# Kernel optimization log

Hardware: AMD Instinct MI355X
Metric: run time of the kernel (lower is better)

Reference implementation:

```python
import jax, jax.numpy as jnp
import numpy as np

B, G, P, H = 32, 5000, 5000, 64
N = B * G
E_CO, E_GG = 1600000, 100000

def _bn(x, g, b):
    # BatchNorm1d in training mode: biased batch stats, eps=1e-5
    m = x.mean(0); v = x.var(0)
    return g * (x - m) * jax.lax.rsqrt(v + 1e-5) + b

def _renorm(t):
    # nn.Embedding(max_norm=True) -> rows renormed to L2 norm <= 1
    n = jnp.linalg.norm(t, axis=1, keepdims=True)
    return t * jnp.minimum(1.0, 1.0 / jnp.maximum(n, 1e-12))

def _sgconv(x, src, dst, w, W, b):
    # SGConv(K=1): gcn_norm (self-loops w=1, symmetric deg norm) spmm, then Linear
    n = x.shape[0]
    sl = jnp.arange(n)
    s = jnp.concatenate([src, sl]); d = jnp.concatenate([dst, sl])
    ww = jnp.concatenate([w, jnp.ones((n,), x.dtype)])
    deg = jax.ops.segment_sum(ww, d, num_segments=n)
    dinv = jnp.where(deg > 0, jax.lax.rsqrt(deg), 0.0)
    coef = dinv[s] * ww * dinv[d]
    agg = jax.ops.segment_sum(coef[:, None] * x[s], d, num_segments=n)
    return agg @ W.T + b

def _mlp3(x, W, b, g, bt):
    # MLP([h,h,h]): Lin-BN-ReLU-Lin-BN (trailing ReLU stripped by [:-1])
    h = jax.nn.relu(_bn(x @ W[0].T + b[0], g[0], bt[0]))
    return _bn(h @ W[1].T + b[1], g[1], bt[1])

def _gears(x, pert_idx, ei_co, w_co, ei_go, w_go, ei_bg, w_bg,
           gene_tab, pos_tab, go_tab, bg_tab, bn_g, bn_b, sg_W, sg_b,
           mlp_W, mlp_b, mlp_g, mlp_bt,
           rec_W1, rec_b1, rec_g1, rec_bt1, rec_W2, rec_b2, rec_g2, rec_bt2,
           indv_w1, indv_b1,
           cg_W1, cg_b1, cg_g1, cg_bt1, cg_W2, cg_b2, cg_g2, cg_bt2,
           indv_w2, indv_b2):
    nb = pert_idx.shape[0]
    ng = gene_tab.shape[0]
    emb = jnp.tile(_renorm(gene_tab), (nb, 1))                     # [B*G,H]
    base = jax.nn.relu(_bn(emb, bn_g[0], bn_b[0]))                 # bn_emb + emb_trans
    pos = jnp.tile(_renorm(pos_tab), (nb, 1))
    pos = _sgconv(pos, ei_co[0], ei_co[1], w_co, sg_W[0], sg_b[0]) # 1 gene-pos GNN layer, no trailing relu
    base = base + 0.2 * pos
    base = _mlp3(base, mlp_W[1], mlp_b[1], mlp_g[1], mlp_bt[1])    # emb_trans_v2
    pgo = _sgconv(_renorm(go_tab), ei_go[0], ei_go[1], w_go, sg_W[1], sg_b[1])
    pbg = _sgconv(_renorm(bg_tab), ei_bg[0], ei_bg[1], w_bg, sg_W[2], sg_b[2])
    pglob = _mlp3(pgo + pbg, mlp_W[0], mlp_b[0], mlp_g[0], mlp_bt[0])  # pert_emb_comb_trans
    base = base.reshape(nb, ng, -1)
    # one valid pert per graph -> pert_track reduces to a gather; pert_fuse then broadcast-add
    emb_total = _mlp3(pglob[pert_idx], mlp_W[2], mlp_b[2], mlp_g[2], mlp_bt[2])  # [B,H]
    base = base + emb_total[:, None, :]
    base = base.reshape(nb * ng, -1)
    base = jax.nn.relu(_bn(base, bn_g[1], bn_b[1]))                # bn_pert_base + transform
    h = jax.nn.relu(_bn(base @ rec_W1.T + rec_b1, rec_g1, rec_bt1))
    out = _bn(h @ rec_W2.T + rec_b2, rec_g2, rec_bt2).reshape(nb, ng, -1)
    w1 = jnp.einsum('bgh,gh->bg', out, indv_w1) + indv_b1          # per-gene decoder 1
    cg = jax.nn.relu(_bn(w1 @ cg_W1.T + cg_b1, cg_g1, cg_bt1))
    cg = _bn(cg @ cg_W2.T + cg_b2, cg_g2, cg_bt2)                  # cross_gene_state [B,H]
    cat = jnp.concatenate([w1[..., None], jnp.broadcast_to(cg[:, None, :], (nb, ng, cg.shape[-1]))], -1)
    out2 = jnp.einsum('bgk,gk->bg', cat, indv_w2) + indv_b2        # per-gene decoder 2
    return out2 + x.reshape(nb, ng)

def setup_inputs():
    ks = jax.random.split(jax.random.key(0), 48)
    rn = lambda i, sh, s=0.05: jax.random.normal(ks[i], sh, jnp.float32) * s
    return {
        "x": rn(0, (N,), 1.0),
        "pert_idx": jax.random.randint(ks[1], (B,), 0, P),
        "ei_co": jax.random.randint(ks[2], (2, E_CO), 0, N),
        "w_co": jax.random.uniform(ks[3], (E_CO,), jnp.float32),
        "ei_go": jax.random.randint(ks[4], (2, E_GG), 0, P),
        "w_go": jax.random.uniform(ks[5], (E_GG,), jnp.float32),
        "ei_bg": jax.random.randint(ks[6], (2, E_GG), 0, P),
        "w_bg": jax.random.uniform(ks[7], (E_GG,), jnp.float32),
        "gene_tab": rn(8, (G, H), 1.0),
        "pos_tab": rn(9, (G, H), 1.0),
        "go_tab": rn(10, (P, H), 1.0),
        "bg_tab": rn(11, (P, H), 1.0),
        "bn_g": jnp.ones((2, H)), "bn_b": jnp.zeros((2, H)),
        "sg_W": rn(12, (3, H, H)), "sg_b": jnp.zeros((3, H)),
        "mlp_W": rn(13, (3, 2, H, H)), "mlp_b": jnp.zeros((3, 2, H)),
        "mlp_g": jnp.ones((3, 2, H)), "mlp_bt": jnp.zeros((3, 2, H)),
        "rec_W1": rn(14, (2 * H, H)), "rec_b1": jnp.zeros((2 * H,)),
        "rec_g1": jnp.ones((2 * H,)), "rec_bt1": jnp.zeros((2 * H,)),
        "rec_W2": rn(15, (H, 2 * H)), "rec_b2": jnp.zeros((H,)),
        "rec_g2": jnp.ones((H,)), "rec_bt2": jnp.zeros((H,)),
        "indv_w1": rn(16, (G, H)), "indv_b1": rn(17, (G,)),
        "cg_W1": rn(18, (H, G), 0.01), "cg_b1": jnp.zeros((H,)),
        "cg_g1": jnp.ones((H,)), "cg_bt1": jnp.zeros((H,)),
        "cg_W2": rn(19, (H, H)), "cg_b2": jnp.zeros((H,)),
        "cg_g2": jnp.ones((H,)), "cg_bt2": jnp.zeros((H,)),
        "indv_w2": rn(20, (G, H + 1)), "indv_b2": rn(21, (G,)),
    }

def reference(x, pert_idx, ei_co, w_co, ei_go, w_go, ei_bg, w_bg,
              gene_tab, pos_tab, go_tab, bg_tab, bn_g, bn_b, sg_W, sg_b,
              mlp_W, mlp_b, mlp_g, mlp_bt,
              rec_W1, rec_b1, rec_g1, rec_bt1, rec_W2, rec_b2, rec_g2, rec_bt2,
              indv_w1, indv_b1,
              cg_W1, cg_b1, cg_g1, cg_bt1, cg_W2, cg_b2, cg_g2, cg_bt2,
              indv_w2, indv_b2):
    return _gears(x, pert_idx, ei_co, w_co, ei_go, w_go, ei_bg, w_bg,
                  gene_tab, pos_tab, go_tab, bg_tab, bn_g, bn_b, sg_W, sg_b,
                  mlp_W, mlp_b, mlp_g, mlp_bt,
                  rec_W1, rec_b1, rec_g1, rec_bt1, rec_W2, rec_b2, rec_g2, rec_bt2,
                  indv_w1, indv_b1,
                  cg_W1, cg_b1, cg_g1, cg_bt1, cg_W2, cg_b2, cg_g2, cg_bt2,
                  indv_w2, indv_b2)
```

## Files before the change

### kernel.cpp

```cpp
#include <hip/hip_runtime.h>

typedef unsigned int u32;
typedef unsigned short u16;

constexpr int Gn  = 5000;
constexpr int Bn  = 32;
constexpr int Pn  = 5000;
constexpr int Nn  = Bn * Gn;
constexpr int ECO = 1600000;
constexpr int EGG = 100000;
constexpr int NTILES = Nn / 128;
constexpr int PTILES = 40;
constexpr int NBK = 625;
constexpr int EPB2 = ECO / 256;
constexpr int NBE = (EGG + 255) / 256;

constexpr int oS2 = 128;
constexpr int oZERO = 1536;
constexpr int oA1 = 2048, oB1 = 2112, oA2 = 2176, oB2 = 2240;
constexpr int oA4 = 2304, oB4 = 2432;
constexpr int oA5 = 2560, oB5 = 2624;
constexpr int oAG = 2688, oBG = 2752;
constexpr int oAP1 = 2816, oBP1 = 2880, oAP2 = 2944, oBP2 = 3008;
constexpr int oAvec = 3072, oCvec = 3136, oCcP = 3200;
// ... 153 lines not shown
  int sel = blockIdx.x >= nbe;
  int blk = sel ? blockIdx.x - nbe : blockIdx.x;
  const int* dst = sel ? dB : dA;
  int* cnt = sel ? cB : cA;
  int* tick = sel ? tB : tA;
  int e = blk * 256 + threadIdx.x;
  if (e < E) tick[e] = atomicAdd(&cnt[dst[e]], 1);
}

__global__ __launch_bounds__(256) void kscan1m(const int* __restrict__ cA, const int* __restrict__ cB,
                                               int* __restrict__ bsA, int* __restrict__ bsB, int n, int nblk) {
  __shared__ int sh[256];
  int sel = blockIdx.x >= nblk;
  int b = sel ? blockIdx.x - nblk : blockIdx.x;
  const int* cnt = sel ? cB : cA;
  int* bsum = sel ? bsB : bsA;
  int t = threadIdx.x;
  int base = b * 1024 + t * 4;
  int s = 0;
#pragma unroll
  for (int j = 0; j < 4; j++) { int i = base + j; if (i < n) s += cnt[i]; }
  sh[t] = s; __syncthreads();
  for (int d = 128; d; d >>= 1) { if (t < d) sh[t] += sh[t + d]; __syncthreads(); }
  if (t == 0) bsum[b] = sh[0];
}

__global__ __launch_bounds__(256) void kscan2m(int* __restrict__ bsA, int* __restrict__ bsB, int nb,
                                               int* __restrict__ totA, int* __restrict__ totB) {
  __shared__ int sh[256];
  int t = threadIdx.x;
  int sel = t >> 7, lt = t & 127;
  int* bsum = sel ? bsB : bsA;
  int v = (lt < nb) ? bsum[lt] : 0;
  sh[t] = v;
  __syncthreads();
  for (int d = 1; d < 128; d <<= 1) {
    int u = (lt >= d) ? sh[t - d] : 0;
    __syncthreads();
    sh[t] += u;
    __syncthreads();
  }
  if (lt < nb) bsum[lt] = sh[t] - v;
  if (lt == nb - 1) *(sel ? totB : totA) = sh[t];
}

__global__ __launch_bounds__(256) void kscan3m(int* __restrict__ cA, int* __restrict__ cB,
                                               const int* __restrict__ bsA, const int* __restrict__ bsB,
                                               int n, int nblk) {
  __shared__ int sh[256];
  int sel = blockIdx.x >= nblk;
  int b = sel ? blockIdx.x - nblk : blockIdx.x;
  int* cnt = sel ? cB : cA;
  const int* bsum = sel ? bsB : bsA;
  int t = threadIdx.x;
  int base = b * 1024 + t * 4;
  int c0 = (base + 0 < n) ? cnt[base + 0] : 0;
  int c1 = (base + 1 < n) ? cnt[base + 1] : 0;
  int c2 = (base + 2 < n) ? cnt[base + 2] : 0;
  int c3 = (base + 3 < n) ? cnt[base + 3] : 0;
  int tot = c0 + c1 + c2 + c3;
  sh[t] = tot; __syncthreads();
  for (int d = 1; d < 256; d <<= 1) {
    int v = (t >= d) ? sh[t - d] : 0;
    __syncthreads();
    sh[t] += v;
    __syncthreads();
  }
  int excl = sh[t] - tot + bsum[b];
  if (base + 0 < n) cnt[base + 0] = excl;
  if (base + 1 < n) cnt[base + 1] = excl + c0;
  if (base + 2 < n) cnt[base + 2] = excl + c0 + c1;
  if (base + 3 < n) cnt[base + 3] = excl + c0 + c1 + c2;
}

__global__ __launch_bounds__(256) void kfilltm(const int* __restrict__ sA, const int* __restrict__ dA,
                                               const float* __restrict__ wA, const int* __restrict__ oA,
                                               const int* __restrict__ tA, float2* __restrict__ pA,
                                               const int* __restrict__ sB, const int* __restrict__ dB,
                                               const float* __restrict__ wB, const int* __restrict__ oB,
                                               const int* __restrict__ tB, float2* __restrict__ pB,
                                               int E, int nbe) {
  int sel = blockIdx.x >= nbe;
  int blk = sel ? blockIdx.x - nbe : blockIdx.x;
  const int* src = sel ? sB : sA;
  const int* dst = sel ? dB : dA;
  const float* w = sel ? wB : wA;
  const int* off = sel ? oB : oA;
  const int* tick = sel ? tB : tA;
  float2* pack = sel ? pB : pA;
  int e = blk * 256 + threadIdx.x;
  if (e >= E) return;
  int d = dst[e];
  pack[off[d] + tick[e]] = make_float2(w[e], __int_as_float(src[e]));
}

__global__ __launch_bounds__(256) void kdinvrowm(const int* __restrict__ oA, const float2* __restrict__ pA,
                                                 float* __restrict__ vA, const int* __restrict__ oB,
                                                 const float2* __restrict__ pB, float* __restrict__ vB,
                                                 int n, int nbe) {
  int sel = blockIdx.x >= nbe;
  int blk = sel ? blockIdx.x - nbe : blockIdx.x;
  const int* off = sel ? oB : oA;
  const float2* pack = sel ? pB : pA;
  float* dinv = sel ? vB : vA;
  int i = blk * 256 + threadIdx.x;
  if (i >= n) return;
  int b0 = off[i], b1 = off[i + 1];
  float s = 1.f;
  for (int j = b0; j < b1; j++) s += pack[j].x;
  dinv[i] = rsqrtf(s);
}

__global__ __launch_bounds__(256) void kgatherm(const int* __restrict__ oA, const float2* __restrict__ pA,
                                                const float* __restrict__ vA, const float* __restrict__ tA,
                                                const int* __restrict__ oB, const float2* __restrict__ pB,
                                                const float* __restrict__ vB, const float* __restrict__ tB,
                                                u16* __restrict__ aggb, int n, int halfBlocks) {
  int sel = blockIdx.x >= halfBlocks;
  int blk = sel ? blockIdx.x - halfBlocks : blockIdx.x;
  const int* off = sel ? oB : oA;
  const float2* pack = sel ? pB : pA;
  const float* dinv = sel ? vB : vA;
  const float* tab = sel ? tB : tA;
  int coff = sel ? 64 : 0;
  int lane = threadIdx.x & 63;
  int wvv = blk * 4 + (threadIdx.x >> 6);
  int nw = halfBlocks * 4;
  for (int i = wvv; i < n; i += nw) {
    int b0 = off[i], b1 = off[i + 1];
    float di = dinv[i];
    float acc = di * tab[(i % Gn) * 64 + lane];
    for (int base = b0; base < b1; base += 64) {
      int m = b1 - base; if (m > 64) m = 64;
      float cj = 0.f; int idxj = 0;
      if (lane < m) {
        float2 p = pack[base + lane];
        int s = __float_as_int(p.y) & 0x3FFFF;
        cj = p.x * dinv[s];
        idxj = (s % Gn) * 64;
      }
      int j = 0;
      for (; j + 1 < m; j += 2) {
        float c0 = __shfl(cj, j, 64);     int i0 = __shfl(idxj, j, 64);
        float c1 = __shfl(cj, j + 1, 64); int i1 = __shfl(idxj, j + 1, 64);
        float t0 = tab[i0 + lane];
        float t1 = tab[i1 + lane];
        acc = fmaf(c0, t0, acc);
        acc = fmaf(c1, t1, acc);
      }
      if (j < m) {
        float c0 = __shfl(cj, j, 64); int i0 = __shfl(idxj, j, 64);
        acc = fmaf(c0, tab[i0 + lane], acc);
      }
    }
    acc *= di;
    aggb[(size_t)i * 128 + coff + lane] = f2bf(acc);
  }
}

__global__ __launch_bounds__(256) void kpsort(const int* __restrict__ src, const int* __restrict__ dst,
                                              const float* __restrict__ w, float2* __restrict__ stg,
                                              int* __restrict__ Cg, int* __restrict__ Lg) {
  __shared__ int cnt[NBK];
  __shared__ int loff[NBK];
  __shared__ int cur[NBK];
  __shared__ int ssc[256];
  __shared__ float2 sbuf[EPB2];
  int t = threadIdx.x;
  int e0 = blockIdx.x * EPB2;
  for (int i = t; i < NBK; i += 256) cnt[i] = 0;
  __syncthreads();
  for (int e = e0 + t; e < e0 + EPB2; e += 256) atomicAdd(&cnt[dst[e] >> 8], 1);
  __syncthreads();
  int i0 = t * 3;
  int c3[3];
  int s = 0;
#pragma unroll
  for (int j = 0; j < 3; j++) { int i = i0 + j; c3[j] = (i < NBK) ? cnt[i] : 0; s += c3[j]; }
  ssc[t] = s;
  __syncthreads();
  for (int d = 1; d < 256; d <<= 1) {
    int u = (t >= d) ? ssc[t - d] : 0;
    __syncthreads();
    ssc[t] += u;
    __syncthreads();
  }
  int base = ssc[t] - s;
#pragma unroll
  for (int j = 0; j < 3; j++) {
    int i = i0 + j;
    if (i < NBK) { loff[i] = base; cur[i] = base; }
    base += c3[j];
  }
  __syncthreads();
  for (int e = e0 + t; e < e0 + EPB2; e += 256) {
    int d = dst[e];
    int pos = atomicAdd(&cur[d >> 8], 1);
    sbuf[pos] = make_float2(w[e], __int_as_float(src[e] | ((d & 255) << 18)));
  }
  __syncthreads();
  for (int i = t; i < EPB2; i += 256) stg[(size_t)e0 + i] = sbuf[i];
  for (int i = t; i < NBK; i += 256) {
    Cg[blockIdx.x * NBK + i] = cnt[i];
    Lg[blockIdx.x * NBK + i] = loff[i];
  }
}

__global__ __launch_bounds__(256) void ksumT(const int* __restrict__ Cg, int* __restrict__ T) {
  int bk = blockIdx.x * 256 + threadIdx.x;
  if (bk >= NBK) return;
  int s = 0;
  for (int blk = 0; blk < 256; blk++) s += Cg[blk * NBK + bk];
  T[bk] = s;
}

__global__ __launch_bounds__(256) void kpscan(const int* __restrict__ bcnt, int* __restrict__ bbase,
                                              int* __restrict__ offN) {
  __shared__ int sh[256];
  int t = threadIdx.x;
  int i0 = t * 3;
  int c[3];
  int s = 0;
#pragma unroll
  for (int j = 0; j < 3; j++) { int i = i0 + j; c[j] = (i < NBK) ? bcnt[i] : 0; s += c[j]; }
  sh[t] = s;
  __syncthreads();
  for (int d = 1; d < 256; d <<= 1) {
    int u = (t >= d) ? sh[t - d] : 0;
    __syncthreads();
    sh[t] += u;
    __syncthreads();
  }
  int base = sh[t] - s;
#pragma unroll
  for (int j = 0; j < 3; j++) {
    int i = i0 + j;
    if (i < NBK) bbase[i] = base;
    base += c[j];
  }
  if (t == 255) { bbase[NBK] = base; *offN = base; }
}

__global__ __launch_bounds__(256) void kpcsr2(const int* __restrict__ bbase, const int* __restrict__ Cg,
                                              const int* __restrict__ Lg, const float2* __restrict__ stg,
                                              int* __restrict__ off, float2* __restrict__ pack,
                                              float* __restrict__ dinv) {
  constexpr int CAP = 4096;
  __shared__ float2 ebuf[CAP];
  __shared__ int rh[256];
  __shared__ int sc2[256];
  __shared__ float ws[256];
  __shared__ int nEs;
  int bk = blockIdx.x, t = threadIdx.x;
  int myC = Cg[t * NBK + bk];
  int myL = Lg[t * NBK + bk];
  sc2[t] = myC;
  __syncthreads();
  for (int d = 1; d < 256; d <<= 1) {
    int u = (t >= d) ? sc2[t - d] : 0;
    __syncthreads();
    sc2[t] += u;
    __syncthreads();
  }
  int myO = sc2[t] - myC;
  if (t == 255) nEs = sc2[255];
  rh[t] = 0; ws[t] = 0.f;
  __syncthreads();
  int nE = nEs;
  {
    const float2* sp = &stg[(size_t)t * EPB2 + myL];
    for (int i = 0; i < myC; i++) ebuf[myO + i] = sp[i];
  }
  __syncthreads();
  for (int i = t; i < nE; i += 256) {
    float2 p = ebuf[i];
    int r = (__float_as_int(p.y) >> 18) & 255;
    atomicAdd(&rh[r], 1);
    atomicAdd(&ws[r], p.x);
  }
  __syncthreads();
  int cnt = rh[t];
  sc2[t] = cnt;
  __syncthreads();
  for (int d = 1; d < 256; d <<= 1) {
    int u = (t >= d) ? sc2[t - d] : 0;
    __syncthreads();
    sc2[t] += u;
    __syncthreads();
  }
  int gpos = bbase[bk] + sc2[t] - cnt;
  int grow = (bk << 8) + t;
  off[grow] = gpos;
  dinv[grow] = rsqrtf(1.f + ws[t]);
  rh[t] = gpos;
  __syncthreads();
  for (int i = t; i < nE; i += 256) {
    float2 p = ebuf[i];
    int r = (__float_as_int(p.y) >> 18) & 255;
    int pos = atomicAdd(&rh[r], 1);
    pack[pos] = p;
  }
}

__global__ __launch_bounds__(256) void kgt3(const int* __restrict__ off, const float2* __restrict__ pack,
                                            const float* __restrict__ dinv, const uint4* __restrict__ PMB,
                                            const float4* __restrict__ Q4, u16* __restrict__ Ybf,
                                            float* __restrict__ partS) {
  __shared__ float sstat[128];
  int t = threadIdx.x;
  int lane = t & 63, wvv = t >> 6;
  int grp = lane >> 3, le = lane & 7;
  for (int idx = t; idx < 128; idx += 256) sstat[idx] = 0.f;
  __syncthreads();
  float sS[8], sQ[8];
#pragma unroll
  for (int j = 0; j < 8; j++) { sS[j] = 0.f; sQ[j] = 0.f; }
  int base0 = (blockIdx.x * 4 + wvv) * 16;
  int stride = gridDim.x * 64;
  for (int i0 = base0; i0 < Nn; i0 += stride) {
    int iA = i0 + grp, iB = i0 + 8 + grp;
    int gA = iA % Gn, gB = iB % Gn;
    int a0 = off[iA], a1 = off[iA + 1];
    int b0 = off[iB], b1 = off[iB + 1];
    float diA = dinv[iA], diB = dinv[iB];
    float accA[8], accB[8];
    {
      uint4 tA = PMB[gA * 8 + le];
      uint4 tB = PMB[gB * 8 + le];
      accA[0] = diA * bflo(tA.x); accA[1] = diA * bfhi(tA.x);
      accA[2] = diA * bflo(tA.y); accA[3] = diA * bfhi(tA.y);
      accA[4] = diA * bflo(tA.z); accA[5] = diA * bfhi(tA.z);
      accA[6] = diA * bflo(tA.w); accA[7] = diA * bfhi(tA.w);
      accB[0] = diB * bflo(tB.x); accB[1] = diB * bfhi(tB.x);
      accB[2] = diB * bflo(tB.y); accB[3] = diB * bfhi(tB.y);
      accB[4] = diB * bflo(tB.z); accB[5] = diB * bfhi(tB.z);
      accB[6] = diB * bflo(tB.w); accB[7] = diB * bfhi(tB.w);
    }
    int curA = a0, curB = b0;
    while (curA < a1 || curB < b1) {
      int mA = a1 - curA; mA = mA > 8 ? 8 : (mA < 0 ? 0 : mA);
      int mB = b1 - curB; mB = mB > 8 ? 8 : (mB < 0 ? 0 : mB);
      float cjA = 0.f, cjB = 0.f; int ixA = 0, ixB = 0;
      if (le < mA) {
        float2 p = pack[curA + le];
        int s = __float_as_int(p.y) & 0x3FFFF;
        cjA = p.x * dinv[s];
        ixA = s % Gn;
      }
      if (le < mB) {
        float2 p = pack[curB + le];
        int s = __float_as_int(p.y) & 0x3FFFF;
        cjB = p.x * dinv[s];
        ixB = s % Gn;
      }
#pragma unroll
      for (int e = 0; e < 8; e++) {
        float cA = __shfl(cjA, grp * 8 + e, 64); int xA = __shfl(ixA, grp * 8 + e, 64);
        float cB = __shfl(cjB, grp * 8 + e, 64); int xB = __shfl(ixB, grp * 8 + e, 64);
        if (e < mA) {
          uint4 tv = PMB[xA * 8 + le];
          accA[0] = fmaf(cA, bflo(tv.x), accA[0]); accA[1] = fmaf(cA, bfhi(tv.x), accA[1]);
          accA[2] = fmaf(cA, bflo(tv.y), accA[2]); accA[3] = fmaf(cA, bfhi(tv.y), accA[3]);
          accA[4] = fmaf(cA, bflo(tv.z), accA[4]); accA[5] = fmaf(cA, bfhi(tv.z), accA[5]);
          accA[6] = fmaf(cA, bflo(tv.w), accA[6]); accA[7] = fmaf(cA, bfhi(tv.w), accA[7]);
        }
        if (e < mB) {
          uint4 tv = PMB[xB * 8 + le];
          accB[0] = fmaf(cB, bflo(tv.x), accB[0]); accB[1] = fmaf(cB, bfhi(tv.x), accB[1]);
          accB[2] = fmaf(cB, bflo(tv.y), accB[2]); accB[3] = fmaf(cB, bfhi(tv.y), accB[3]);
          accB[4] = fmaf(cB, bflo(tv.z), accB[4]); accB[5] = fmaf(cB, bfhi(tv.z), accB[5]);
          accB[6] = fmaf(cB, bflo(tv.w), accB[6]); accB[7] = fmaf(cB, bfhi(tv.w), accB[7]);
        }
      }
      curA += mA; curB += mB;
    }
    {
      float4 q0 = Q4[gA * 16 + le * 2];
      float4 q1 = Q4[gA * 16 + le * 2 + 1];
      float v[8];
      v[0] = fmaf(diA, accA[0], q0.x); v[1] = fmaf(diA, accA[1], q0.y);
      v[2] = fmaf(diA, accA[2], q0.z); v[3] = fmaf(diA, accA[3], q0.w);
      v[4] = fmaf(diA, accA[4], q1.x); v[5] = fmaf(diA, accA[5], q1.y);
      v[6] = fmaf(diA, accA[6], q1.z); v[7] = fmaf(diA, accA[7], q1.w);
#pragma unroll
      for (int j = 0; j < 8; j++) { sS[j] += v[j]; sQ[j] += v[j] * v[j]; }
      uint4 o;
      o.x = (u32)f2bf(v[0]) | ((u32)f2bf(v[1]) << 16);
      o.y = (u32)f2bf(v[2]) | ((u32)f2bf(v[3]) << 16);
      o.z = (u32)f2bf(v[4]) | ((u32)f2bf(v[5]) << 16);
      o.w = (u32)f2bf(v[6]) | ((u32)f2bf(v[7]) << 16);
      *(uint4*)&Ybf[(size_t)iA * 64 + le * 8] = o;
    }
    {
      float4 q0 = Q4[gB * 16 + le * 2];
      float4 q1 = Q4[gB * 16 + le * 2 + 1];
      float v[8];
      v[0] = fmaf(diB, accB[0], q0.x); v[1] = fmaf(diB, accB[1], q0.y);
      v[2] = fmaf(diB, accB[2], q0.z); v[3] = fmaf(diB, accB[3], q0.w);
      v[4] = fmaf(diB, accB[4], q1.x); v[5] = fmaf(diB, accB[5], q1.y);
      v[6] = fmaf(diB, accB[6], q1.z); v[7] = fmaf(diB, accB[7], q1.w);
#pragma unroll
      for (int j = 0; j < 8; j++) { sS[j] += v[j]; sQ[j] += v[j] * v[j]; }
      uint4 o;
      o.x = (u32)f2bf(v[0]) | ((u32)f2bf(v[1]) << 16);
      o.y = (u32)f2bf(v[2]) | ((u32)f2bf(v[3]) << 16);
      o.z = (u32)f2bf(v[4]) | ((u32)f2bf(v[5]) << 16);
      o.w = (u32)f2bf(v[6]) | ((u32)f2bf(v[7]) << 16);
      *(uint4*)&Ybf[(size_t)iB * 64 + le * 8] = o;
    }
  }
#pragma unroll
  for (int j = 0; j < 8; j++) {
    atomicAdd(&sstat[le * 8 + j], sS[j]);
    atomicAdd(&sstat[64 + le * 8 + j], sQ[j]);
  }
  __syncthreads();
  for (int idx = t; idx < 128; idx += 256) partS[(size_t)blockIdx.x * 128 + idx] = sstat[idx];
}

template <int K, int OUTC, bool PRE, bool EB, bool PERG, bool STATS, bool OUTF32, bool STATB>
__global__ __launch_bounds__(256, 3) void mfgemm(
    const u16* __restrict__ Xb, const float* __restrict__ Wg, const float* __restrict__ bias,
    const float* __restrict__ pa, const float* __restrict__ pb,
    const float* __restrict__ perg, u16* __restrict__ Ybf, float* __restrict__ stats,
    float* __restrict__ statB, int rows) {
  constexpr int NT  = OUTC / 16;
  constexpr int KH  = K / 32;
  constexpr int SLK = K / 8;
  constexpr int SLO = OUTC / 8;
  constexpr int XROW = (K > OUTC ? K : OUTC) * 2;
  __shared__ __align__(16) unsigned char xsb[128 * XROW];
  __shared__ __align__(16) unsigned char wsb[OUTC * K * 2];
  __shared__ float sstat[STATS ? 2 * OUTC : 1];
  __shared__ float sstatB[STATB ? 128 : 1];
  int t = threadIdx.x;
  int l = t & 63, w = t >> 6, lrow = l & 15, lk = l >> 4;
  int R0 = blockIdx.x * 128;

  for (int idx = t; idx < OUTC * SLK; idx += 256) {
    int oc = idx / SLK, s8 = idx % SLK;
    const float* wp = &Wg[oc * K + s8 * 8];
    uint4 o;
    o.x = (u32)f2bf(wp[0]) | ((u32)f2bf(wp[1]) << 16);
    o.y = (u32)f2bf(wp[2]) | ((u32)f2bf(wp[3]) << 16);
    o.z = (u32)f2bf(wp[4]) | ((u32)f2bf(wp[5]) << 16);
    o.w = (u32)f2bf(wp[6]) | ((u32)f2bf(wp[7]) << 16);
    *(uint4*)&wsb[oc * (2 * K) + ((s8 * 16) ^ ((oc & 7) << 4))] = o;
  }
  if constexpr (STATS) for (int idx = t; idx < 2 * OUTC; idx += 256) sstat[idx] = 0.f;
  if constexpr (STATB) for (int idx = t; idx < 128; idx += 256) sstatB[idx] = 0.f;

#pragma unroll
  for (int m = 0; m < SLK / 2; m++) {
    int f = m * 256 + t;
    int r = f / SLK, s8 = f % SLK;
    uint4 u = *(const uint4*)&Xb[(size_t)(R0 + r) * K + s8 * 8];
    if constexpr (PRE) {
      int c0 = s8 * 8;
      float4 A0 = *(const float4*)&pa[c0];
      float4 A1 = *(const float4*)&pa[c0 + 4];
      const float* pbb = EB ? &pb[((R0 + r) / Gn) * 64] : pb;
      float4 B0 = *(const float4*)&pbb[c0];
      float4 B1 = *(const float4*)&pbb[c0 + 4];
      float v0 = fmaxf(fmaf(A0.x, bflo(u.x), B0.x), 0.f);
      float v1 = fmaxf(fmaf(A0.y, bfhi(u.x), B0.y), 0.f);
      float v2 = fmaxf(fmaf(A0.z, bflo(u.y), B0.z), 0.f);
      float v3 = fmaxf(fmaf(A0.w, bfhi(u.y), B0.w), 0.f);
      float v4 = fmaxf(fmaf(A1.x, bflo(u.z), B1.x), 0.f);
      float v5 = fmaxf(fmaf(A1.y, bfhi(u.z), B1.y), 0.f);
      float v6 = fmaxf(fmaf(A1.z, bflo(u.w), B1.z), 0.f);
      float v7 = fmaxf(fmaf(A1.w, bfhi(u.w), B1.w), 0.f);
      u.x = (u32)f2bf(v0) | ((u32)f2bf(v1) << 16);
      u.y = (u32)f2bf(v2) | ((u32)f2bf(v3) << 16);
      u.z = (u32)f2bf(v4) | ((u32)f2bf(v5) << 16);
      u.w = (u32)f2bf(v6) | ((u32)f2bf(v7) << 16);
    }
    *(uint4*)&xsb[r * XROW + ((s8 * 16) ^ ((r & 7) << 4))] = u;
  }
  float bcol[NT];
#pragma unroll
  for (int nt = 0; nt < NT; nt++) bcol[nt] = bias[nt * 16 + lrow];
  __syncthreads();

  short8v af[2][KH];
#pragma unroll
  for (int rt = 0; rt < 2; rt++)
#pragma unroll
    for (int h = 0; h < KH; h++) {
      int row = w * 32 + rt * 16 + lrow;
      af[rt][h] = *(const short8v*)&xsb[row * XROW + ((h * 64 + lk * 16) ^ ((row & 7) << 4))];
    }
  f32x4 acc[2][NT];
#pragma unroll
  for (int rt = 0; rt < 2; rt++)
#pragma unroll
    for (int nt = 0; nt < NT; nt++) {
      f32x4 z = {0.f, 0.f, 0.f, 0.f};
      acc[rt][nt] = z;
    }
#pragma unroll
  for (int nt = 0; nt < NT; nt++) {
    int brow = nt * 16 + lrow;
#pragma unroll
    for (int h = 0; h < KH; h++) {
      short8v bfr = *(const short8v*)&wsb[brow * (2 * K) + ((h * 64 + lk * 16) ^ ((brow & 7) << 4))];
      acc[0][nt] = __builtin_amdgcn_mfma_f32_16x16x32_bf16(af[0][h], bfr, acc[0][nt], 0, 0, 0);
      acc[1][nt] = __builtin_amdgcn_mfma_f32_16x16x32_bf16(af[1][h], bfr, acc[1][nt], 0, 0, 0);
    }
  }
  __syncthreads();

  float sS[NT], sQ[NT], sB0[NT], sB1[NT];
#pragma unroll
  for (int nt = 0; nt < NT; nt++) { sS[nt] = 0.f; sQ[nt] = 0.f; sB0[nt] = 0.f; sB1[nt] = 0.f; }
  int hiStart = STATB ? (R0 / Gn + 1) * Gn : 0x7fffffff;
  float* Yf = (float*)Ybf;
#pragma unroll
  for (int rt = 0; rt < 2; rt++) {
#pragma unroll
    for (int r = 0; r < 4; r++) {
      int orow = w * 32 + rt * 16 + lk * 4 + r;
      int grow = R0 + orow;
      bool valid = grow < rows;
      int qoff = 0;
      if constexpr (PERG) qoff = (grow % Gn) * 64;
#pragma unroll
      for (int nt = 0; nt < NT; nt++) {
        float v = acc[rt][nt][r] + bcol[nt];
        if constexpr (PERG) v += perg[qoff + nt * 16 + lrow];
        if (valid) {
          if constexpr (STATS) { sS[nt] += v; sQ[nt] += v * v; }
          if constexpr (STATB) { if (grow >= hiStart) sB1[nt] += v; else sB0[nt] += v; }
        }
        if constexpr (OUTF32) {
          if (valid) Yf[(size_t)grow * OUTC + nt * 16 + lrow] = v;
        } else {
          *(u16*)&xsb[orow * (2 * OUTC) + ((2 * (nt * 16 + lrow)) ^ ((orow & 7) << 4))] = f2bf(v);
        }
      }
    }
  }
  if constexpr (STATS) {
#pragma unroll
    for (int nt = 0; nt < NT; nt++) {
      atomicAdd(&sstat[nt * 16 + lrow], sS[nt]);
      atomicAdd(&sstat[OUTC + nt * 16 + lrow], sQ[nt]);
    }
  }
  if constexpr (STATB) {
#pragma unroll
    for (int nt = 0; nt < NT; nt++) {
      atomicAdd(&sstatB[nt * 16 + lrow], sB0[nt]);
      atomicAdd(&sstatB[64 + nt * 16 + lrow], sB1[nt]);
    }
  }
  __syncthreads();

  if constexpr (!OUTF32) {
#pragma unroll
    for (int m = 0; m < SLO / 2; m++) {
      int f = m * 256 + t;
      int r = f / SLO, c8 = f % SLO;
      uint4 o = *(const uint4*)&xsb[r * (2 * OUTC) + ((16 * c8) ^ ((r & 7) << 4))];
      *(uint4*)&Ybf[(size_t)(R0 + r) * OUTC + c8 * 8] = o;
    }
  }
  if constexpr (STATS)
    for (int idx = t; idx < 2 * OUTC; idx += 256) stats[(size_t)blockIdx.x * 2 * OUTC + idx] = sstat[idx];
  if constexpr (STATB)
    for (int idx = t; idx < 128; idx += 256) statB[(size_t)blockIdx.x * 128 + idx] = sstatB[idx];
}

__global__ __launch_bounds__(256) void kfinS3e2(const float* __restrict__ S2, const float* __restrict__ g,
                                                const float* __restrict__ bt, const float* __restrict__ a2,
                                                const float* __restrict__ b2, const float* __restrict__ emb,
                                                const float* __restrict__ S3B,
                                                float* __restrict__ Avec, float* __restrict__ e2) {
  __shared__ float a3s[64], b3s[64];
  int t = threadIdx.x;
  if (t < 64) {
    float a2c = a2[t], b2c = b2[t];
    float su = 0.f, sxc = 0.f, sc2 = 0.f;
    for (int b = 0; b < Bn; b++) {
      float cb = b2c + emb[b * 64 + t];
      float sb = S3B[b * 64 + t];
      su += cb;
      sxc += cb * sb;
      sc2 += cb * cb;
    }
    float Su = a2c * S2[t] + (float)Gn * su;
    float Sq = a2c * a2c * S2[64 + t] + 2.f * a2c * sxc + (float)Gn * sc2;
    float mean = Su * (1.f / Nn);
    float var = Sq * (1.f / Nn) - mean * mean;
    float sc = g[t] * rsqrtf(var + 1e-5f);
    float sh = bt[t] - mean * sc;
    a3s[t] = sc; b3s[t] = sh;
    Avec[t] = sc * a2c;
  }
  __syncthreads();
  for (int idx = t; idx < 2048; idx += 256) {
    int c = idx & 63;
    e2[idx] = a3s[c] * (b2[c] + emb[idx]) + b3s[c];
  }
}

__global__ __launch_bounds__(256) void k13_kernel(const u16* __restrict__ R2, const float* __restrict__ a5,
                                                  const float* __restrict__ b5, const float* __restrict__ iw1,
                                                  const float* __restrict__ ib1, float* __restrict__ w1out,
                                                  int rows) {
  int t = blockIdx.x * 256 + threadIdx.x;
  int i = t >> 4, j = t & 15;
  if (i >= rows) return;
  int g = i % Gn;
  uint2 u = *(const uint2*)&R2[(size_t)i * 64 + j * 4];
  float rx = bflo(u.x), ry = bfhi(u.x), rz = bflo(u.y), rw = bfhi(u.y);
  float4 a = ((const float4*)a5)[j];
  float4 b = ((const float4*)b5)[j];
  float4 w = ((const float4*)iw1)[g * 16 + j];
  float p = (a.x * rx + b.x) * w.x + (a.y * ry + b.y) * w.y +
            (a.z * rz + b.z) * w.z + (a.w * rw + b.w) * w.w;
  for (int off = 8; off; off >>= 1) p += __shfl_xor(p, off, 64);
  if (j == 0) w1out[i] = p + ib1[g];
}

__global__ __launch_bounds__(256) void kinitcg(const float* __restrict__ cgb1, float* __restrict__ cgraw) {
  int idx = blockIdx.x * 256 + threadIdx.x;
  if (idx < Bn * 64) cgraw[idx] = cgb1[idx & 63];
}

__global__ __launch_bounds__(256) void kcg1s(const float* __restrict__ w1, const float* __restrict__ cgW1,
                                             float* __restrict__ cgraw) {
  __shared__ float w1s[64 * 36];
  __shared__ float cgs[64 * 65];
  int t = threadIdx.x;
  int k0 = blockIdx.x * 64;
  int kmax = Gn - k0; if (kmax > 64) kmax = 64;
  for (int idx = t; idx < 2048; idx += 256) {
    int row = idx >> 6, k = idx & 63;
    w1s[k * 36 + row] = (k < kmax) ? w1[row * Gn + k0 + k] : 0.f;
  }
  for (int idx = t; idx < 4096; idx += 256) {
    int col = idx >> 6, k = idx & 63;
    cgs[k * 65 + col] = (k < kmax) ? cgW1[col * Gn + k0 + k] : 0.f;
  }
  __syncthreads();
  int col = t & 63, rg = t >> 6;
  float acc[8];
#pragma unroll
  for (int i = 0; i < 8; i++) acc[i] = 0.f;
  for (int k = 0; k < 64; k++) {
    float wk = cgs[k * 65 + col];
    const float* wr = &w1s[k * 36 + rg * 8];
    float4 r0 = *(const float4*)wr;
    float4 r1 = *(const float4*)(wr + 4);
    acc[0] = fmaf(r0.x, wk, acc[0]);
    acc[1] = fmaf(r0.y, wk, acc[1]);
    acc[2] = fmaf(r0.z, wk, acc[2]);
    acc[3] = fmaf(r0.w, wk, acc[3]);
    acc[4] = fmaf(r1.x, wk, acc[4]);
    acc[5] = fmaf(r1.y, wk, acc[5]);
    acc[6] = fmaf(r1.z, wk, acc[6]);
    acc[7] = fmaf(r1.w, wk, acc[7]);
  }
#pragma unroll
  for (int i = 0; i < 8; i++) atomicAdd(&cgraw[(rg * 8 + i) * 64 + col], acc[i]);
}

__global__ __launch_bounds__(256) void kcg2(const float* __restrict__ cgraw, const float* __restrict__ g1,
                                            const float* __restrict__ bt1, const float* __restrict__ W2,
                                            const float* __restrict__ b2, const float* __restrict__ g2,
                                            const float* __restrict__ bt2, float* __restrict__ cg2out) {
  int t = threadIdx.x, c = t & 63, bg = t >> 6;
  __shared__ float hmid[2048], sred[4][64], qred[4][64], asc[64], bsh[64];
  float y[8];
  float ps = 0.f, pq = 0.f;
  for (int jb = 0; jb < 8; jb++) {
    int b = bg * 8 + jb;
    float v = cgraw[b * 64 + c];
    y[jb] = v; ps += v; pq += v * v;
  }
  sred[bg][c] = ps; qred[bg][c] = pq;
  __syncthreads();
  if (t < 64) {
    float s = sred[0][t] + sred[1][t] + sred[2][t] + sred[3][t];
    float q = qred[0][t] + qred[1][t] + qred[2][t] + qred[3][t];
    float mean = s * (1.f / 32.f), var = q * (1.f / 32.f) - mean * mean;
    float sc = g1[t] * rsqrtf(var + 1e-5f);
    asc[t] = sc; bsh[t] = bt1[t] - mean * sc;
  }
  __syncthreads();
  for (int jb = 0; jb < 8; jb++) { int b = bg * 8 + jb; hmid[b * 64 + c] = fmaxf(asc[c] * y[jb] + bsh[c], 0.f); }
  __syncthreads();
  ps = 0.f; pq = 0.f;
  for (int jb = 0; jb < 8; jb++) {
    int b = bg * 8 + jb;
    float a = b2[c];
    for (int k = 0; k < 64; k++) a += hmid[b * 64 + k] * W2[c * 64 + k];
    y[jb] = a; ps += a; pq += a * a;
  }
  sred[bg][c] = ps; qred[bg][c] = pq;
  __syncthreads();
  if (t < 64) {
    float s = sred[0][t] + sred[1][t] + sred[2][t] + sred[3][t];
    float q = qred[0][t] + qred[1][t] + qred[2][t] + qred[3][t];
    float mean = s * (1.f / 32.f), var = q * (1.f / 32.f) - mean * mean;
    float sc = g2[t] * rsqrtf(var + 1e-5f);
    asc[t] = sc; bsh[t] = bt2[t] - mean * sc;
  }
  __syncthreads();
  for (int jb = 0; jb < 8; jb++) { int b = bg * 8 + jb; cg2out[b * 64 + c] = asc[c] * y[jb] + bsh[c]; }
}

__global__ __launch_bounds__(256) void kemb(const u16* __restrict__ m2, const float* __restrict__ aP2,
                                            const float* __restrict__ bP2, const int* __restrict__ pidx,
                                            const float* __restrict__ Wm, const float* __restrict__ bv,
                                            const float* __restrict__ gg, const float* __restrict__ btv,
                                            float* __restrict__ emb) {
  int t = threadIdx.x, c = t & 63, bg = t >> 6;
  __shared__ float xin[2048], hmid[2048], sred[4][64], qred[4][64], asc[64], bsh[64];
  for (int idx = t; idx < 2048; idx += 256) {
    int b = idx >> 6, cc = idx & 63;
    xin[idx] = aP2[cc] * bf2f(m2[(size_t)pidx[b] * 64 + cc]) + bP2[cc];
  }
  __syncthreads();
  float y[8];
  float ps = 0.f, pq = 0.f;
  for (int jb = 0; jb < 8; jb++) {
    int b = bg * 8 + jb;
    float a = bv[c];
    for (int k = 0; k < 64; k++) a += xin[b * 64 + k] * Wm[c * 64 + k];
    y[jb] = a; ps += a; pq += a * a;
  }
  sred[bg][c] = ps; qred[bg][c] = pq;
  __syncthreads();
  if (t < 64) {
    float s = sred[0][t] + sred[1][t] + sred[2][t] + sred[3][t];
    float q = qred[0][t] + qred[1][t] + qred[2][t] + qred[3][t];
    float mean = s * (1.f / 32.f), var = q * (1.f / 32.f) - mean * mean;
    float sc = gg[t] * rsqrtf(var + 1e-5f);
    asc[t] = sc; bsh[t] = btv[t] - mean * sc;
  }
  __syncthreads();
  for (int jb = 0; jb < 8; jb++) { int b = bg * 8 + jb; hmid[b * 64 + c] = fmaxf(asc[c] * y[jb] + bsh[c], 0.f); }
  __syncthreads();
  ps = 0.f; pq = 0.f;
  for (int jb = 0; jb < 8; jb++) {
    int b = bg * 8 + jb;
    float a = bv[64 + c];
    for (int k = 0; k < 64; k++) a += hmid[b * 64 + k] * Wm[4096 + c * 64 + k];
    y[jb] = a; ps += a; pq += a * a;
  }
  sred[bg][c] = ps; qred[bg][c] = pq;
  __syncthreads();
  if (t < 64) {
    float s = sred[0][t] + sred[1][t] + sred[2][t] + sred[3][t];
    float q = qred[0][t] + qred[1][t] + qred[2][t] + qred[3][t];
    float mean = s * (1.f / 32.f), var = q * (1.f / 32.f) - mean * mean;
    float sc = gg[64 + t] * rsqrtf(var + 1e-5f);
    asc[t] = sc; bsh[t] = btv[64 + t] - mean * sc;
  }
  __syncthreads();
  for (int jb = 0; jb < 8; jb++) { int b = bg * 8 + jb; emb[b * 64 + c] = asc[c] * y[jb] + bsh[c]; }
}

__global__ __launch_bounds__(256) void kfinal(const float* __restrict__ w1, const float* __restrict__ cg2,
                                              const float* __restrict__ iw2, const float* __restrict__ ib2,
                                              const float* __restrict__ x, float* __restrict__ out) {
  __shared__ float iws[64 * 65], cgs[2048];
  int t = threadIdx.x;
  int g0 = blockIdx.x * 64;
  for (int idx = t; idx < 64 * 65; idx += 256) {
    int gi = g0 * 65 + idx;
    iws[idx] = (gi < Gn * 65) ? iw2[gi] : 0.f;
  }
  for (int idx = t; idx < 2048; idx += 256) cgs[idx] = cg2[idx];
  __syncthreads();
  int gl = t & 63, bg = t >> 6;
  int g = g0 + gl;
  if (g >= Gn) return;
  float bias = ib2[g];
  for (int jb = 0; jb < 8; jb++) {
    int b = bg * 8 + jb;
    float acc = w1[b * Gn + g] * iws[gl * 65] + bias;
    for (int k = 0; k < 64; k++) acc += cgs[b * 64 + k] * iws[gl * 65 + 1 + k];
    out[b * Gn + g] = acc + x[b * Gn + g];
  }
}

extern "C" void kernel_launch(void* const* d_in, const int* in_sizes, int n_in,
                              void* d_out, int out_size, void* d_ws, size_t ws_size,
                              hipStream_t stream) {
  (void)in_sizes; (void)n_in; (void)out_size;
  if (ws_size < WS_FLOATS * sizeof(float)) return;

  const float* x        = (const float*)d_in[0];
  const int*   pert_idx = (const int*)d_in[1];
  const int*   ei_co    = (const int*)d_in[2];
  const float* w_co     = (const float*)d_in[3];
  const int*   ei_go    = (const int*)d_in[4];
  const float* w_go     = (const float*)d_in[5];
  const int*   ei_bg    = (const int*)d_in[6];
  const float* w_bg     = (const float*)d_in[7];
  const float* gene_tab = (const float*)d_in[8];
  const float* pos_tab  = (const float*)d_in[9];
  const float* go_tab   = (const float*)d_in[10];
  const float* bg_tab   = (const float*)d_in[11];
  const float* bn_g     = (const float*)d_in[12];
  const float* bn_b     = (const float*)d_in[13];
  const float* sg_W     = (const float*)d_in[14];
  const float* sg_b     = (const float*)d_in[15];
  const float* mlp_W    = (const float*)d_in[16];
  const float* mlp_b    = (const float*)d_in[17];
  const float* mlp_g    = (const float*)d_in[18];
  const float* mlp_bt   = (const float*)d_in[19];
  const float* rec_W1   = (const float*)d_in[20];
  const float* rec_b1   = (const float*)d_in[21];
  const float* rec_g1   = (const float*)d_in[22];
  const float* rec_bt1  = (const float*)d_in[23];
  const float* rec_W2   = (const float*)d_in[24];
  const float* rec_b2   = (const float*)d_in[25];
  const float* rec_g2   = (const float*)d_in[26];
  const float* rec_bt2  = (const float*)d_in[27];
  const float* indv_w1  = (const float*)d_in[28];
  const float* indv_b1  = (const float*)d_in[29];
  const float* cg_W1    = (const float*)d_in[30];
  const float* cg_b1    = (const float*)d_in[31];
  const float* cg_g1    = (const float*)d_in[32];
  const float* cg_bt1   = (const float*)d_in[33];
  const float* cg_W2    = (const float*)d_in[34];
  const float* cg_b2    = (const float*)d_in[35];
  const float* cg_g2    = (const float*)d_in[36];
  const float* cg_bt2   = (const float*)d_in[37];
  const float* indv_w2  = (const float*)d_in[38];
  const float* indv_b2  = (const float*)d_in[39];

  float* W = (float*)d_ws;
  float* buf0 = W + oBUF0;
  float* buf1 = W + oBUF1;

  int*    co_off    = (int*)(buf1);
  int*    bbase     = (int*)(buf1 + 200000);
  int*    Tbk       = (int*)(buf1 + 202000);
  int*    sbsum     = (int*)(buf1 + 320128);
  float2* co_pack   = (float2*)(buf1 + 400000);
  int*    go_cnt    = (int*)(buf1 + 3700000);
  float2* go_pack   = (float2*)(buf1 + 3720000);
  int*    bg_cnt    = (int*)(buf1 + 4000000);
  float2* bg_pack   = (float2*)(buf1 + 4020000);
  u16*    RPB       = (u16*)(buf1 + 4220000);
  int*    Cg        = (int*)(buf1 + 4500000);
  int*    Lg        = (int*)(buf1 + 4700000);
  int*    go_ticket = (int*)(buf1 + 6200000);
  int*    bg_ticket = (int*)(buf1 + 6400000);
  u16*    pgi       = (u16*)(buf1 + 6600000);
  u16*    RGB       = (u16*)(buf1 + 6800000);
  float2* co_stg    = (float2*)(buf1 + 6963840);

  float* partS = buf1 + 8000000;
  float* partB = buf1 + 8650000;

  kzero4<<<30, 256, 0, stream>>>(W, 2048,
                                 buf1 + 6800000 + 160000, 3840,
                                 buf1 + 4220000 + 160000, 3840,
                                 buf1 + 6600000 + 320000, 7680);
  krenorm4<<<640, 256, 0, stream>>>(gene_tab, pos_tab, go_tab, bg_tab,
                                    W + oRG, W + oRP, W + oRGO, W + oRBG,
                                    RGB, RPB, partS);
  kredfin<<<1, 1024, 0, stream>>>(partS, 160, 64, bn_g, bn_b, W + oAG, W + oBG, nullptr, 1.f / Gn);
  ksmallmat<<<1, 256, 0, stream>>>(mlp_W + 8192, sg_W, 0.2f, mlp_b + 128, sg_b, nullptr, 0.2f,
                                   W + oM, 64, W + oCvec);
  ksmallmat<<<1, 256, 0, stream>>>(mlp_W, sg_W + 4096, 1.f, nullptr, nullptr, nullptr, 0.f,
                                   W + oM1, 128, nullptr);
  ksmallmat<<<1, 256, 0, stream>>>(mlp_W, sg_W + 8192, 1.f, mlp_b, sg_b + 64, sg_b + 128, 1.f,
                                   W + oM1 + 64, 128, W + oCcP);
  mfgemm<64, 64, true, false, false, false, true, false><<<PTILES, 256, 0, stream>>>(
      RGB, mlp_W + 8192, W + oCvec, W + oAG, W + oBG, nullptr, (u16*)(W + oQ), nullptr, nullptr, Gn);
  mfgemm<64, 64, false, false, false, false, false, false><<<PTILES, 256, 0, stream>>>(
      RPB, W + oM, W + oZERO, nullptr, nullptr, nullptr, (u16*)(W + oPM), nullptr, nullptr, Gn);

  kzero2<<<20, 256, 0, stream>>>(go_cnt, bg_cnt, 5001);
  khist2<<<2 * NBE, 256, 0, stream>>>(ei_go + EGG, go_cnt, go_ticket,
                                      ei_bg + EGG, bg_cnt, bg_ticket, EGG, NBE);
  kscan1m<<<10, 256, 0, stream>>>(go_cnt, bg_cnt, sbsum, sbsum + 64, Pn, 5);
  kscan2m<<<1, 256, 0, stream>>>(sbsum, sbsum + 64, 5, go_cnt + Pn, bg_cnt + Pn);
  kscan3m<<<10, 256, 0, stream>>>(go_cnt, bg_cnt, sbsum, sbsum + 64, Pn, 5);
  kfilltm<<<2 * NBE, 256, 0, stream>>>(ei_go, ei_go + EGG, w_go, go_cnt, go_ticket, go_pack,
                                       ei_bg, ei_bg + EGG, w_bg, bg_cnt, bg_ticket, bg_pack, EGG, NBE);
  kdinvrowm<<<40, 256, 0, stream>>>(go_cnt, go_pack, W + oDGO, bg_cnt, bg_pack, W + oDBG, Pn, 20);
  kgatherm<<<1024, 256, 0, stream>>>(go_cnt, go_pack, W + oDGO, W + oRGO,
                                     bg_cnt, bg_pack, W + oDBG, W + oRBG, pgi, Pn, 512);

  mfgemm<128, 64, false, false, false, true, false, false><<<PTILES, 256, 0, stream>>>(
      pgi, W + oM1, W + oCcP, nullptr, nullptr, nullptr, (u16*)(W + oM1B), partS, nullptr, Pn);
  kredfin<<<1, 1024, 0, stream>>>(partS, PTILES, 64, mlp_g, mlp_bt, W + oAP1, W + oBP1, nullptr, 1.f / Pn);
  mfgemm<64, 64, true, false, false, true, false, false><<<PTILES, 256, 0, stream>>>(
      (u16*)(W + oM1B), mlp_W + 4096, mlp_b + 64, W + oAP1, W + oBP1, nullptr,
      (u16*)(W + oM2B), partS, nullptr, Pn);
  kredfin<<<1, 1024, 0, stream>>>(partS, PTILES, 64, mlp_g + 64, mlp_bt + 64, W + oAP2, W + oBP2, nullptr, 1.f / Pn);
  kemb<<<1, 256, 0, stream>>>((u16*)(W + oM2B), W + oAP2, W + oBP2, pert_idx,
                              mlp_W + 16384, mlp_b + 256, mlp_g + 256, mlp_bt + 256, W + oEMB);

  kpsort<<<256, 256, 0, stream>>>(ei_co, ei_co + ECO, w_co, co_stg, Cg, Lg);
  ksumT<<<3, 256, 0, stream>>>(Cg, Tbk);
  kpscan<<<1, 256, 0, stream>>>(Tbk, bbase, co_off + Nn);
  kpcsr2<<<NBK, 256, 0, stream>>>(bbase, Cg, Lg, co_stg, co_off, co_pack, W + oDEG);

  kgt3<<<2048, 256, 0, stream>>>(co_off, co_pack, W + oDEG, (const uint4*)(W + oPM),
                                 (const float4*)(W + oQ), (u16*)buf0, partS);
  kredfin<<<1, 1024, 0, stream>>>(partS, 2048, 64, mlp_g + 128, mlp_bt + 128, W + oA1, W + oB1, nullptr, 1.f / Nn);

  mfgemm<64, 64, true, false, false, true, false, true><<<NTILES, 256, 0, stream>>>(
      (const u16*)buf0, mlp_W + 12288, mlp_b + 192, W + oA1, W + oB1, nullptr,
      (u16*)buf1, partS, partB, Nn);
  kredfin<<<1, 1024, 0, stream>>>(partS, NTILES, 64, mlp_g + 192, mlp_bt + 192, W + oA2, W + oB2, W + oS2, 1.f / Nn);
  kredB<<<32, 64, 0, stream>>>(partB, W + oE2);
  kfinS3e2<<<1, 256, 0, stream>>>(W + oS2, bn_g + 64, bn_b + 64, W + oA2, W + oB2, W + oEMB,
                                  W + oE2, W + oAvec, W + oE2);
  mfgemm<64, 128, true, true, false, true, false, false><<<NTILES, 256, 0, stream>>>(
      (const u16*)buf1, rec_W1, rec_b1, W + oAvec, W + oE2, nullptr, (u16*)buf0, partS, nullptr, Nn);
  kredfin<<<2, 1024, 0, stream>>>(partS, NTILES, 128, rec_g1, rec_bt1, W + oA4, W + oB4, nullptr, 1.f / Nn);
  mfgemm<128, 64, true, false, false, true, false, false><<<NTILES, 256, 0, stream>>>(
      (const u16*)buf0, rec_W2, rec_b2, W + oA4, W + oB4, nullptr, (u16*)buf1, partS, nullptr, Nn);
  kredfin<<<1, 1024, 0, stream>>>(partS, NTILES, 64, rec_g2, rec_bt2, W + oA5, W + oB5, nullptr, 1.f / Nn);
  k13_kernel<<<(Nn * 16 + 255) / 256, 256, 0, stream>>>((const u16*)buf1, W + oA5, W + oB5, indv_w1, indv_b1,
                                                        W + oW1, Nn);
  kinitcg<<<8, 256, 0, stream>>>(cg_b1, W + oCGRAW);
  kcg1s<<<(Gn + 63) / 64, 256, 0, stream>>>(W + oW1, cg_W1, W + oCGRAW);
  kcg2<<<1, 256, 0, stream>>>(W + oCGRAW, cg_g1, cg_bt1, cg_W2, cg_b2, cg_g2, cg_bt2, W + oCG2);
  kfinal<<<(Gn + 63) / 64, 256, 0, stream>>>(W + oW1, W + oCG2, indv_w2, indv_b2, x, (float*)d_out);
}
```

Before: 705.0 us.

## Gather co-expression SpMM one row per wave with fp32 projected table

The SpMM gather kernel now assigns one destination row to each 64-lane wave instead of two rows per 8-lane group. Four quarter-waves each take a different edge, every edge loads a float4 slice from an fp32 projected table, and partial sums are combined with xor shuffles. The table producer switches to fp32 output to support this, which doubles gather bytes per edge but removes the bf16 unpacking. Batch-norm statistics are reduced through shared arrays instead of shared atomics. The risk is lower row-level parallelism per wave and wasted lanes on rows with few edges.

```diff
diff --git a/kernel.cpp b/kernel.cpp
--- a/kernel.cpp
+++ b/kernel.cpp
@@ -479,120 +479,79 @@
   }
 }
 
-__global__ __launch_bounds__(256) void kgt3(const int* __restrict__ off, const float2* __restrict__ pack,
-                                            const float* __restrict__ dinv, const uint4* __restrict__ PMB,
+__global__ __launch_bounds__(256) void kgt1(const int* __restrict__ off, const float2* __restrict__ pack,
+                                            const float* __restrict__ dinv, const float4* __restrict__ PM4,
                                             const float4* __restrict__ Q4, u16* __restrict__ Ybf,
                                             float* __restrict__ partS) {
-  __shared__ float sstat[128];
+  __shared__ float sred[4][64], sqred[4][64];
   int t = threadIdx.x;
   int lane = t & 63, wvv = t >> 6;
-  int grp = lane >> 3, le = lane & 7;
-  for (int idx = t; idx < 128; idx += 256) sstat[idx] = 0.f;
-  __syncthreads();
-  float sS[8], sQ[8];
-#pragma unroll
-  for (int j = 0; j < 8; j++) { sS[j] = 0.f; sQ[j] = 0.f; }
-  int base0 = (blockIdx.x * 4 + wvv) * 16;
-  int stride = gridDim.x * 64;
-  for (int i0 = base0; i0 < Nn; i0 += stride) {
-    int iA = i0 + grp, iB = i0 + 8 + grp;
-    int gA = iA % Gn, gB = iB % Gn;
-    int a0 = off[iA], a1 = off[iA + 1];
-    int b0 = off[iB], b1 = off[iB + 1];
-    float diA = dinv[iA], diB = dinv[iB];
-    float accA[8], accB[8];
-    {
-      uint4 tA = PMB[gA * 8 + le];
-      uint4 tB = PMB[gB * 8 + le];
-      accA[0] = diA * bflo(tA.x); accA[1] = diA * bfhi(tA.x);
-      accA[2] = diA * bflo(tA.y); accA[3] = diA * bfhi(tA.y);
-      accA[4] = diA * bflo(tA.z); accA[5] = diA * bfhi(tA.z);
-      accA[6] = diA * bflo(tA.w); accA[7] = diA * bfhi(tA.w);
-      accB[0] = diB * bflo(tB.x); accB[1] = diB * bfhi(tB.x);
-      accB[2] = diB * bflo(tB.y); accB[3] = diB * bfhi(tB.y);
-      accB[4] = diB * bflo(tB.z); accB[5] = diB * bfhi(tB.z);
-      accB[6] = diB * bflo(tB.w); accB[7] = diB * bfhi(tB.w);
-    }
-    int curA = a0, curB = b0;
-    while (curA < a1 || curB < b1) {
-      int mA = a1 - curA; mA = mA > 8 ? 8 : (mA < 0 ? 0 : mA);
-      int mB = b1 - curB; mB = mB > 8 ? 8 : (mB < 0 ? 0 : mB);
-      float cjA = 0.f, cjB = 0.f; int ixA = 0, ixB = 0;
-      if (le < mA) {
-        float2 p = pack[curA + le];
+  int q = lane >> 4, kq = lane & 15;
+  int gw = blockIdx.x * 4 + wvv, nw = gridDim.x * 4;
+  float4 sS = make_float4(0.f, 0.f, 0.f, 0.f);
+  float4 sQ = make_float4(0.f, 0.f, 0.f, 0.f);
+  for (int i = gw; i < Nn; i += nw) {
+    int g = i % Gn;
+    int b0 = off[i], b1 = off[i + 1];
+    float di = dinv[i];
+    float4 acc = make_float4(0.f, 0.f, 0.f, 0.f);
+    if (q == 0) {
+      float4 pm = PM4[g * 16 + kq];
+      acc.x = di * pm.x; acc.y = di * pm.y; acc.z = di * pm.z; acc.w = di * pm.w;
+    }
+    for (int base = b0; base < b1; base += 64) {
+      int m = b1 - base; if (m > 64) m = 64;
+      float cj = 0.f; int idx16 = 0;
+      if (lane < m) {
+        float2 p = pack[base + lane];
         int s = __float_as_int(p.y) & 0x3FFFF;
-        cjA = p.x * dinv[s];
-        ixA = s % Gn;
+        cj = p.x * dinv[s];
+        idx16 = (s % Gn) * 16;
       }
-      if (le < mB) {
-        float2 p = pack[curB + le];
-        int s = __float_as_int(p.y) & 0x3FFFF;
-        cjB = p.x * dinv[s];
-        ixB = s % Gn;
-      }
-#pragma unroll
-      for (int e = 0; e < 8; e++) {
-        float cA = __shfl(cjA, grp * 8 + e, 64); int xA = __shfl(ixA, grp * 8 + e, 64);
-        float cB = __shfl(cjB, grp * 8 + e, 64); int xB = __shfl(ixB, grp * 8 + e, 64);
-        if (e < mA) {
-          uint4 tv = PMB[xA * 8 + le];
-          accA[0] = fmaf(cA, bflo(tv.x), accA[0]); accA[1] = fmaf(cA, bfhi(tv.x), accA[1]);
-          accA[2] = fmaf(cA, bflo(tv.y), accA[2]); accA[3] = fmaf(cA, bfhi(tv.y), accA[3]);
-          accA[4] = fmaf(cA, bflo(tv.z), accA[4]); accA[5] = fmaf(cA, bfhi(tv.z), accA[5]);
-          accA[6] = fmaf(cA, bflo(tv.w), accA[6]); accA[7] = fmaf(cA, bfhi(tv.w), accA[7]);
-        }
-        if (e < mB) {
-          uint4 tv = PMB[xB * 8 + le];
-          accB[0] = fmaf(cB, bflo(tv.x), accB[0]); accB[1] = fmaf(cB, bfhi(tv.x), accB[1]);
-          accB[2] = fmaf(cB, bflo(tv.y), accB[2]); accB[3] = fmaf(cB, bfhi(tv.y), accB[3]);
-          accB[4] = fmaf(cB, bflo(tv.z), accB[4]); accB[5] = fmaf(cB, bfhi(tv.z), accB[5]);
-          accB[6] = fmaf(cB, bflo(tv.w), accB[6]); accB[7] = fmaf(cB, bfhi(tv.w), accB[7]);
+      int steps = (m + 3) >> 2;
+      for (int st = 0; st < steps; st++) {
+        int e = st * 4 + q;
+        float c = __shfl(cj, e, 64);
+        int ix = __shfl(idx16, e, 64);
+        if (e < m) {
+          float4 tv = PM4[ix + kq];
+          acc.x = fmaf(c, tv.x, acc.x);
+          acc.y = fmaf(c, tv.y, acc.y);
+          acc.z = fmaf(c, tv.z, acc.z);
+          acc.w = fmaf(c, tv.w, acc.w);
         }
       }
-      curA += mA; curB += mB;
-    }
-    {
-      float4 q0 = Q4[gA * 16 + le * 2];
-      float4 q1 = Q4[gA * 16 + le * 2 + 1];
-      float v[8];
-      v[0] = fmaf(diA, accA[0], q0.x); v[1] = fmaf(diA, accA[1], q0.y);
-      v[2] = fmaf(diA, accA[2], q0.z); v[3] = fmaf(diA, accA[3], q0.w);
-      v[4] = fmaf(diA, accA[4], q1.x); v[5] = fmaf(diA, accA[5], q1.y);
-      v[6] = fmaf(diA, accA[6], q1.z); v[7] = fmaf(diA, accA[7], q1.w);
-#pragma unroll
-      for (int j = 0; j < 8; j++) { sS[j] += v[j]; sQ[j] += v[j] * v[j]; }
-      uint4 o;
-      o.x = (u32)f2bf(v[0]) | ((u32)f2bf(v[1]) << 16);
-      o.y = (u32)f2bf(v[2]) | ((u32)f2bf(v[3]) << 16);
-      o.z = (u32)f2bf(v[4]) | ((u32)f2bf(v[5]) << 16);
-      o.w = (u32)f2bf(v[6]) | ((u32)f2bf(v[7]) << 16);
-      *(uint4*)&Ybf[(size_t)iA * 64 + le * 8] = o;
-    }
-    {
-      float4 q0 = Q4[gB * 16 + le * 2];
-      float4 q1 = Q4[gB * 16 + le * 2 + 1];
-      float v[8];
-      v[0] = fmaf(diB, accB[0], q0.x); v[1] = fmaf(diB, accB[1], q0.y);
-      v[2] = fmaf(diB, accB[2], q0.z); v[3] = fmaf(diB, accB[3], q0.w);
-      v[4] = fmaf(diB, accB[4], q1.x); v[5] = fmaf(diB, accB[5], q1.y);
-      v[6] = fmaf(diB, accB[6], q1.z); v[7] = fmaf(diB, accB[7], q1.w);
-#pragma unroll
-      for (int j = 0; j < 8; j++) { sS[j] += v[j]; sQ[j] += v[j] * v[j]; }
-      uint4 o;
-      o.x = (u32)f2bf(v[0]) | ((u32)f2bf(v[1]) << 16);
-      o.y = (u32)f2bf(v[2]) | ((u32)f2bf(v[3]) << 16);
-      o.z = (u32)f2bf(v[4]) | ((u32)f2bf(v[5]) << 16);
-      o.w = (u32)f2bf(v[6]) | ((u32)f2bf(v[7]) << 16);
-      *(uint4*)&Ybf[(size_t)iB * 64 + le * 8] = o;
-    }
-  }
-#pragma unroll
-  for (int j = 0; j < 8; j++) {
-    atomicAdd(&sstat[le * 8 + j], sS[j]);
-    atomicAdd(&sstat[64 + le * 8 + j], sQ[j]);
-  }
-  __syncthreads();
-  for (int idx = t; idx < 128; idx += 256) partS[(size_t)blockIdx.x * 128 + idx] = sstat[idx];
+    }
+    acc.x += __shfl_xor(acc.x, 16, 64); acc.y += __shfl_xor(acc.y, 16, 64);
+    acc.z += __shfl_xor(acc.z, 16, 64); acc.w += __shfl_xor(acc.w, 16, 64);
+    acc.x += __shfl_xor(acc.x, 32, 64); acc.y += __shfl_xor(acc.y, 32, 64);
+    acc.z += __shfl_xor(acc.z, 32, 64); acc.w += __shfl_xor(acc.w, 32, 64);
+    float4 qv = Q4[g * 16 + kq];
+    float4 v;
+    v.x = fmaf(di, acc.x, qv.x); v.y = fmaf(di, acc.y, qv.y);
+    v.z = fmaf(di, acc.z, qv.z); v.w = fmaf(di, acc.w, qv.w);
+    if (q == 0) {
+      sS.x += v.x; sS.y += v.y; sS.z += v.z; sS.w += v.w;
+      sQ.x += v.x * v.x; sQ.y += v.y * v.y; sQ.z += v.z * v.z; sQ.w += v.w * v.w;
+      uint2 o;
+      o.x = (u32)f2bf(v.x) | ((u32)f2bf(v.y) << 16);
+      o.y = (u32)f2bf(v.z) | ((u32)f2bf(v.w) << 16);
+      *(uint2*)&Ybf[(size_t)i * 64 + kq * 4] = o;
+    }
+  }
+  if (q == 0) {
+    sred[wvv][kq * 4 + 0] = sS.x; sred[wvv][kq * 4 + 1] = sS.y;
+    sred[wvv][kq * 4 + 2] = sS.z; sred[wvv][kq * 4 + 3] = sS.w;
+    sqred[wvv][kq * 4 + 0] = sQ.x; sqred[wvv][kq * 4 + 1] = sQ.y;
+    sqred[wvv][kq * 4 + 2] = sQ.z; sqred[wvv][kq * 4 + 3] = sQ.w;
+  }
+  __syncthreads();
+  if (t < 64) {
+    float s = sred[0][t] + sred[1][t] + sred[2][t] + sred[3][t];
+    float qq = sqred[0][t] + sqred[1][t] + sqred[2][t] + sqred[3][t];
+    partS[(size_t)blockIdx.x * 128 + t] = s;
+    partS[(size_t)blockIdx.x * 128 + 64 + t] = qq;
+  }
 }
 
 template <int K, int OUTC, bool PRE, bool EB, bool PERG, bool STATS, bool OUTF32, bool STATB>
@@ -1052,7 +1011,7 @@
                                    W + oM1 + 64, 128, W + oCcP);
   mfgemm<64, 64, true, false, false, false, true, false><<<PTILES, 256, 0, stream>>>(
       RGB, mlp_W + 8192, W + oCvec, W + oAG, W + oBG, nullptr, (u16*)(W + oQ), nullptr, nullptr, Gn);
-  mfgemm<64, 64, false, false, false, false, false, false><<<PTILES, 256, 0, stream>>>(
+  mfgemm<64, 64, false, false, false, false, true, false><<<PTILES, 256, 0, stream>>>(
       RPB, W + oM, W + oZERO, nullptr, nullptr, nullptr, (u16*)(W + oPM), nullptr, nullptr, Gn);
 
   kzero2<<<20, 256, 0, stream>>>(go_cnt, bg_cnt, 5001);
@@ -1082,7 +1041,7 @@
   kpscan<<<1, 256, 0, stream>>>(Tbk, bbase, co_off + Nn);
   kpcsr2<<<NBK, 256, 0, stream>>>(bbase, Cg, Lg, co_stg, co_off, co_pack, W + oDEG);
 
-  kgt3<<<2048, 256, 0, stream>>>(co_off, co_pack, W + oDEG, (const uint4*)(W + oPM),
+  kgt1<<<2048, 256, 0, stream>>>(co_off, co_pack, W + oDEG, (const float4*)(W + oPM),
                                  (const float4*)(W + oQ), (u16*)buf0, partS);
   kredfin<<<1, 1024, 0, stream>>>(partS, 2048, 64, mlp_g + 128, mlp_bt + 128, W + oA1, W + oB1, nullptr, 1.f / Nn);
 
```

New measurement: 687.7 us. 2.5% less time.
